# Optimization experiments

Hardware: AMD Instinct MI355X
Metric: run time of the kernel (lower is better)

## Reference

```python
import jax, jax.numpy as jnp
import numpy as np


def conv3x3(x, w):
    # x: [B,C,H,W], w: [O,I,3,3], stride 1, pad 1, no bias
    return jax.lax.conv_general_dilated(
        x, w, window_strides=(1, 1), padding=[(1, 1), (1, 1)],
        dimension_numbers=("NCHW", "OIHW", "NCHW"))


def deform_conv2d(x, offset, w):
    """torchvision-style DeformConv2d: k=3, stride=1, pad=1, dilation=1,
    1 offset group, no bias. x:[B,C,H,W], offset:[B,18,H,W] (dy,dx pairs
    per kernel tap, k = kh*3+kw), w:[O,C,3,3]. Zero padding outside."""
    B, C, H, W = x.shape
    K = 9
    dy = offset[:, 0::2]  # [B,9,H,W]
    dx = offset[:, 1::2]
    kh = (jnp.arange(K) // 3 - 1).astype(x.dtype)[None, :, None, None]
    kw = (jnp.arange(K) % 3 - 1).astype(x.dtype)[None, :, None, None]
    hh = jnp.arange(H, dtype=x.dtype)[None, None, :, None]
    ww = jnp.arange(W, dtype=x.dtype)[None, None, None, :]
    py = hh + kh + dy  # sampling y coord, [B,9,H,W]
    px = ww + kw + dx
    y0 = jnp.floor(py)
    x0 = jnp.floor(px)
    wy = py - y0
    wx = px - x0
    x_hwc = jnp.transpose(x, (0, 2, 3, 1))  # [B,H,W,C]
    b_idx = jnp.arange(B)[:, None, None, None]

    def gather(yi, xi):
        valid = (yi >= 0) & (yi <= H - 1) & (xi >= 0) & (xi <= W - 1)
        yc = jnp.clip(yi, 0, H - 1).astype(jnp.int32)
        xc = jnp.clip(xi, 0, W - 1).astype(jnp.int32)
        v = x_hwc[b_idx, yc, xc]  # [B,9,H,W,C]
        return v * valid[..., None].astype(x.dtype)

    v00 = gather(y0, x0)
    v01 = gather(y0, x0 + 1)
    v10 = gather(y0 + 1, x0)
    v11 = gather(y0 + 1, x0 + 1)
    wy = wy[..., None]
    wx = wx[..., None]
    sampled = (v00 * (1 - wy) * (1 - wx) + v01 * (1 - wy) * wx
               + v10 * wy * (1 - wx) + v11 * wy * wx)  # [B,9,H,W,C]
    wk = w.reshape(w.shape[0], w.shape[1], K)  # [O,C,9]
    return jnp.einsum("bkhwc,ock->bohw", sampled, wk)


def setup_inputs() -> dict:
    key = jax.random.key(0)
    ks = jax.random.split(key, 6)
    B, C, H, W = 2, 128, 128, 128
    s = 0.05  # small init so learned offsets stay in a realistic range
    return {
        "input_features": jax.random.normal(ks[0], (B, C, H, W), jnp.float32),
        "reference_features": jax.random.normal(ks[1], (B, C, H, W), jnp.float32),
        "w_est1": jax.random.normal(ks[2], (C, 2 * C, 3, 3), jnp.float32) * s,
        "w_est2": jax.random.normal(ks[3], (C, C, 3, 3), jnp.float32) * s,
        "w_off": jax.random.normal(ks[4], (18, C, 3, 3), jnp.float32) * s,
        "w_def": jax.random.normal(ks[5], (C, C, 3, 3), jnp.float32) * s,
    }


def reference(input_features, reference_features, w_est1, w_est2, w_off, w_def):
    # concat input+reference features along channel dim
    feat = jnp.concatenate([input_features, reference_features], axis=1)  # [B,2C,H,W]
    # dynamic offset estimator: 2-layer 3x3 conv stack 2C->C->C with ReLU
    est = jax.nn.relu(conv3x3(feat, w_est1))
    est = jax.nn.relu(conv3x3(est, w_est2))
    # offset head: C -> 2*9 offsets per pixel
    offset = conv3x3(est, w_off)  # [B,18,H,W]
    # deformable conv over the reference features
    return deform_conv2d(reference_features, offset, w_def)
```

## Files before the change

kernel.cpp:

```cpp
#include <hip/hip_runtime.h>

typedef _Float16 f16;
typedef __attribute__((ext_vector_type(8))) _Float16 f16x8;
typedef __attribute__((ext_vector_type(4))) float f32x4;

#define H_ 128
#define W_ 128


__device__ __forceinline__ void g2l16(const void* g, void* l) {
  __builtin_amdgcn_global_load_lds((const __attribute__((address_space(1))) void*)g,
                                   (__attribute__((address_space(3))) void*)l, 16, 0, 0);
}

__device__ __forceinline__ void pack_conv(const float* __restrict__ src, f16* __restrict__ dst,
                                          long idx, int C, int NT, int NB, int O) {
  int ci3 = idx & 7;
  int g = (idx >> 3) & 3;
  long t1 = idx >> 5;
  int o = t1 % NT;  long t2 = t1 / NT;
  int kx = t2 % 3;  long t3 = t2 / 3;
  int nb = t3 % NB; long t4 = t3 / NB;
  int nkc = C >> 5;
  int cc = t4 % nkc;
  int ky = t4 / nkc;
  int oo = nb * NT + o;
  int c = (cc << 5) + ((g ^ ((o >> 1) & 3)) << 3) + ci3;
  float v = (oo < O) ? src[(((size_t)oo * C + c) * 3 + ky) * 3 + kx] : 0.f;
  dst[idx] = (f16)v;
}

__device__ __forceinline__ void halo_zero(f16* __restrict__ buf, long e, int C) {
  int c = e & (C - 1);
  long t = e / C;
  int b = (int)(t / 516);
  int p = (int)(t % 516);
  int y, x;
  if (p < 130)      { y = 0;   x = p; }
  else if (p < 260) { y = 129; x = p - 130; }
  else if (p < 388) { x = 0;   y = p - 259; }
  else              { x = 129; y = p - 387; }
  buf[((size_t)(b * 130 + y) * 130 + x) * C + c] = (f16)0.f;
}

__global__ __launch_bounds__(256) void prep_k(const float* __restrict__ w1, const float* __restrict__ w2,
                                              const float* __restrict__ woff, const float* __restrict__ wdef,
                                              f16* __restrict__ W1p, f16* __restrict__ W2p,
                                              f16* __restrict__ Woffp, f16* __restrict__ Wdefp,
                                              f16* __restrict__ featB, f16* __restrict__ est1,
                                              f16* __restrict__ est2) {
  long idx = (long)blockIdx.x * 256 + threadIdx.x;
  if (idx < 294912) { pack_conv(w1, W1p, idx, 256, 64, 2, 128); return; }
  idx -= 294912;
  if (idx < 147456) { pack_conv(w2, W2p, idx, 128, 64, 2, 128); return; }
  idx -= 147456;
  if (idx < 36864) { pack_conv(woff, Woffp, idx, 128, 32, 1, 18); return; }
  idx -= 36864;
  if (idx < 147456) {
    int ci3 = idx & 7;
    int g = (idx >> 3) & 15;
    int o = (idx >> 7) & 127;
    int t = (int)(idx >> 14);
    int c = ((g ^ (o & 7)) << 3) + ci3;
    Wdefp[idx] = (f16)wdef[(((size_t)o * 128 + c) * 3 + t / 3) * 3 + t % 3];
    return;
  }
  idx -= 147456;
  if (idx < 264192) { halo_zero(featB, idx, 256); return; }
  idx -= 264192;
  if (idx < 132096) { halo_zero(est1, idx, 128); return; }
  idx -= 132096;
  if (idx < 132096) halo_zero(est2, idx, 128);
}

__global__ __launch_bounds__(256) void to_nhwc_k(const float* __restrict__ x,
                                                 const float* __restrict__ ref,
                                                 f16* __restrict__ featB) {
  int row = blockIdx.x;
  int b = row >> 7, h = row & 127;
  int w0 = blockIdx.y * 64;
  int chunk = blockIdx.z;
  const float* src = (chunk < 4) ? x : ref;
  int c0 = (chunk & 3) * 32;
  __shared__ __align__(16) f16 T[64][40];
  int tid = threadIdx.x;
#pragma unroll
  for (int i = 0; i < 2; ++i) {
    int idx = tid + i * 256;
    int c = idx >> 4, g = idx & 15;
    const float4 v = *(const float4*)(src + (((size_t)(b * 128 + c0 + c)) * H_ + h) * W_ + w0 + g * 4);
    T[g * 4 + 0][c] = (f16)v.x;
    T[g * 4 + 1][c] = (f16)v.y;
    T[g * 4 + 2][c] = (f16)v.z;
    T[g * 4 + 3][c] = (f16)v.w;
  }
  __syncthreads();
  int w = tid >> 2, g = tid & 3;
  f16x8 o = *(const f16x8*)&T[w][g * 8];
  *(f16x8*)(featB + ((size_t)(b * 130 + h + 1) * 130 + w0 + w + 1) * 256 + chunk * 32 + g * 8) = o;
}

template <int CIN, int NT, bool RELU, bool F16OUT>
__global__ __launch_bounds__(256, 2) void conv_k(const f16* __restrict__ src,
                                                 const f16* __restrict__ Wp,
                                                 f16* __restrict__ dstH,
                                                 float* __restrict__ dstF) {
  const int row = blockIdx.x, nb = blockIdx.y;
  const int b = row >> 7, h = row & 127;
  constexpr int NKC = CIN / 32;
  constexpr int NB = (NT == 64) ? 2 : 1;
  __shared__ __align__(16) f16 As[130][32];
  __shared__ __align__(16) f16 Bs[3][NT][32];
  const int tid = threadIdx.x;
  const int lane = tid & 63, wave = tid >> 6;
  const int l16 = lane & 15, quad = lane >> 4;
  constexpr int MI = (NT == 64) ? 4 : 2;
  const int wmBase = (NT == 64) ? (wave >> 1) * 64 : wave * 32;
  const int wn = (NT == 64) ? (wave & 1) : 0;
  f32x4 acc[MI][2] = {};
  char* AsF = (char*)&As[0][0];
  char* BsF = (char*)&Bs[0][0][0];
  for (int ky = 0; ky < 3; ++ky) {
    const f16* abase0 = src + ((size_t)(b * 130 + h + ky) * 130) * CIN;
    for (int cc = 0; cc < NKC; ++cc) {
      __syncthreads();
      const f16* abase = abase0 + cc * 32;
      {
#pragma unroll
        for (int r = 0; r < 2; ++r) {
          int ch = r * 256 + tid;
          int x = ch >> 2, g = ch & 3;
          g2l16(abase + (size_t)x * CIN + ((g ^ ((x >> 1) & 3)) << 3), AsF + ch * 16);
        }
        if (tid < 8) {
          int ch = 512 + tid;
          int x = ch >> 2, g = ch & 3;
          g2l16(abase + (size_t)x * CIN + ((g ^ ((x >> 1) & 3)) << 3), AsF + ch * 16);
        }
      }
      {
        const f16* bbase = Wp + ((size_t)((ky * NKC + cc) * NB + nb)) * (3 * NT * 32);
        constexpr int BCH = 3 * NT * 32 / 8;
#pragma unroll
        for (int r = 0; r < BCH / 256; ++r) {
          int ch = r * 256 + tid;
          g2l16(bbase + ch * 8, BsF + ch * 16);
        }
        if constexpr (BCH % 256) {
          if (tid < BCH % 256) {
            int ch = (BCH / 256) * 256 + tid;
            g2l16(bbase + ch * 8, BsF + ch * 16);
          }
        }
      }
      __syncthreads();
#pragma unroll
      for (int kx = 0; kx < 3; ++kx) {
        f16x8 bf[2];
#pragma unroll
        for (int j = 0; j < 2; ++j) {
          int o = wn * 32 + j * 16 + l16;
          bf[j] = *(const f16x8*)&Bs[kx][o][(quad ^ ((o >> 1) & 3)) << 3];
        }
#pragma unroll
        for (int i = 0; i < MI; ++i) {
          int x = wmBase + i * 16 + l16 + kx;
          f16x8 a = *(const f16x8*)&As[x][(quad ^ ((x >> 1) & 3)) << 3];
#pragma unroll
          for (int j = 0; j < 2; ++j)
            acc[i][j] = __builtin_amdgcn_mfma_f32_16x16x32_f16(a, bf[j], acc[i][j], 0, 0, 0);
        }
      }
    }
  }
#pragma unroll
  for (int i = 0; i < MI; ++i)
#pragma unroll
    for (int j = 0; j < 2; ++j) {
      int o = nb * NT + wn * 32 + j * 16 + l16;
#pragma unroll
      for (int r = 0; r < 4; ++r) {
        int m = wmBase + i * 16 + quad * 4 + r;
        float v = acc[i][j][r];
        if (RELU) v = fmaxf(v, 0.f);
        if (F16OUT)
          dstH[((size_t)(b * 130 + h + 1) * 130 + m + 1) * 128 + o] = (f16)v;
        else
          dstF[((size_t)row * 128 + m) * 32 + o] = v;
      }
    }
}

__global__ __launch_bounds__(256, 2) void deform_k(const f16* __restrict__ featB,
                                                   const float* __restrict__ offb,
                                                   const f16* __restrict__ Wdefp,
                                                   float* __restrict__ out) {
  const int row = blockIdx.x, tile = blockIdx.y;
  const int b = row >> 7, h = row & 127;
  __shared__ __align__(16) f16 Ws[128][128];
  __shared__ __align__(16) f16 Ss[64][128];
  __shared__ int4 mlds[9][64];
  const int tid = threadIdx.x;
  const int lane = tid & 63, wave = tid >> 6;
  const int l16 = lane & 15, quad = lane >> 4;
  for (int e = tid; e < 576; e += 256) {
    int t = e >> 6, p = e & 63;
    int w = tile * 64 + p;
    const float2 d = *(const float2*)(offb + ((size_t)row * 128 + w) * 32 + 2 * t);
    float py = (float)(h + t / 3 - 1) + d.x;
    float pxf = (float)(w + t % 3 - 1) + d.y;
    float fy = floorf(py), fx = floorf(pxf);
    mlds[t][p] = make_int4((int)fy, (int)fx, __float_as_int(py - fy), __float_as_int(pxf - fx));
  }
  f32x4 acc[2][4] = {};
  const int px = tid >> 2;
  const int cgrp = tid & 3;
  char* WsF = (char*)&Ws[0][0];
  for (int t = 0; t < 9; ++t) {
    __syncthreads();
    const f16* wt = Wdefp + (size_t)t * 16384;
#pragma unroll
    for (int r = 0; r < 8; ++r) {
      int ch = r * 256 + tid;
      g2l16(wt + ch * 8, WsF + ch * 16);
    }
    {
      int4 mt = mlds[t][px];
      int iy = mt.x, ix = mt.y;
      float wy = __int_as_float(mt.z), wx = __int_as_float(mt.w);
      int yp = iy + 1, xp = ix + 1;
      bool y0v = (unsigned)yp < 130u, y1v = (unsigned)(yp + 1) < 130u;
      bool x0v = (unsigned)xp < 130u, x1v = (unsigned)(xp + 1) < 130u;
      int cy0 = y0v ? yp : 0, cy1 = y1v ? yp + 1 : 0;
      int cx0 = x0v ? xp : 0, cx1 = x1v ? xp + 1 : 0;
      float u0 = (1.f - wy) * (y0v ? 1.f : 0.f), u1 = wy * (y1v ? 1.f : 0.f);
      float s0 = (1.f - wx) * (x0v ? 1.f : 0.f), s1 = wx * (x1v ? 1.f : 0.f);
      f16 h00 = (f16)(u0 * s0), h01 = (f16)(u0 * s1);
      f16 h10 = (f16)(u1 * s0), h11 = (f16)(u1 * s1);
      const size_t bb = (size_t)b * 130;
      const f16* p00 = featB + ((bb + cy0) * 130 + cx0) * 256 + 128 + cgrp * 32;
      const f16* p01 = featB + ((bb + cy0) * 130 + cx1) * 256 + 128 + cgrp * 32;
      const f16* p10 = featB + ((bb + cy1) * 130 + cx0) * 256 + 128 + cgrp * 32;
      const f16* p11 = featB + ((bb + cy1) * 130 + cx1) * 256 + 128 + cgrp * 32;
      f16x8 v00[4], v01[4], v10[4], v11[4];
#pragma unroll
      for (int q = 0; q < 4; ++q) {
        v00[q] = *(const f16x8*)(p00 + q * 8);
        v01[q] = *(const f16x8*)(p01 + q * 8);
        v10[q] = *(const f16x8*)(p10 + q * 8);
        v11[q] = *(const f16x8*)(p11 + q * 8);
      }
#pragma unroll
      for (int q = 0; q < 4; ++q) {
        f16x8 rb = v00[q] * h00 + v01[q] * h01 + v10[q] * h10 + v11[q] * h11;
        int c = cgrp * 4 + q;
        *(f16x8*)&Ss[px][(c ^ (px & 7)) << 3] = rb;
      }
    }
    __syncthreads();
#pragma unroll
    for (int cc = 0; cc < 4; ++cc) {
      f16x8 af[2], bf[4];
#pragma unroll
      for (int i = 0; i < 2; ++i) {
        int o = wave * 32 + i * 16 + l16;
        af[i] = *(const f16x8*)&Ws[o][((cc * 4 + quad) ^ (o & 7)) << 3];
      }
#pragma unroll
      for (int j = 0; j < 4; ++j) {
        int p = j * 16 + l16;
        bf[j] = *(const f16x8*)&Ss[p][((cc * 4 + quad) ^ (p & 7)) << 3];
      }
#pragma unroll
      for (int i = 0; i < 2; ++i)
#pragma unroll
        for (int j = 0; j < 4; ++j)
          acc[i][j] = __builtin_amdgcn_mfma_f32_16x16x32_f16(af[i], bf[j], acc[i][j], 0, 0, 0);
    }
  }
#pragma unroll
  for (int i = 0; i < 2; ++i)
#pragma unroll
    for (int r = 0; r < 4; ++r) {
      int o = wave * 32 + i * 16 + quad * 4 + r;
#pragma unroll
      for (int j = 0; j < 4; ++j) {
        int w = tile * 64 + j * 16 + l16;
        out[((size_t)(b * 128 + o) * 128 + h) * 128 + w] = acc[i][j][r];
      }
    }
}

extern "C" void kernel_launch(void* const* d_in, const int* in_sizes, int n_in,
                              void* d_out, int out_size, void* d_ws, size_t ws_size,
                              hipStream_t stream) {
  const float* x = (const float*)d_in[0];
  const float* ref = (const float*)d_in[1];
  const float* w1 = (const float*)d_in[2];
  const float* w2 = (const float*)d_in[3];
  const float* woff = (const float*)d_in[4];
  const float* wdef = (const float*)d_in[5];
  float* out = (float*)d_out;
  char* ws = (char*)d_ws;
  f16* featB = (f16*)(ws + 0);
  f16* est1 = (f16*)(ws + 17305600);
  f16* est2 = (f16*)(ws + 25958400);
  float* offb = (float*)(ws + 34611200);
  f16* W1p = (f16*)(ws + 38805504);
  f16* W2p = (f16*)(ws + 39395328);
  f16* Woffp = (f16*)(ws + 39690240);
  f16* Wdefp = (f16*)(ws + 39763968);

  prep_k<<<dim3(4512), 256, 0, stream>>>(w1, w2, woff, wdef, W1p, W2p, Woffp, Wdefp,
                                         featB, est1, est2);
  to_nhwc_k<<<dim3(256, 2, 8), 256, 0, stream>>>(x, ref, featB);
  conv_k<256, 64, true, true><<<dim3(256, 2), 256, 0, stream>>>(featB, W1p, est1, nullptr);
  conv_k<128, 64, true, true><<<dim3(256, 2), 256, 0, stream>>>(est1, W2p, est2, nullptr);
  conv_k<128, 32, false, false><<<dim3(256, 1), 256, 0, stream>>>(est2, Woffp, nullptr, offb);
  deform_k<<<dim3(256, 2), 256, 0, stream>>>(featB, offb, Wdefp, out);
}
```

Measured before the change: 183.3 us.

## Fuse offset conv into deform kernel, double-buffer convs, merge prep kernels

Merges the NHWC transpose into the weight-prep kernel and removes one launch. The conv kernel is retiled: each block now covers 64 pixels by 128 output channels, with double-buffered LDS staging of activations and weights. The offset-head conv is computed inside the deform kernel with MFMA reading est2 directly, which drops the separate launch and the fp32 offset buffer. The deform kernel splits output channels across a grid z dimension and double-buffers sampling and weight DMA. The trade is that the offset conv is recomputed once per output-channel half, LDS use per block rises, and the offset conv reads its weights straight from global memory.

```diff
diff --git a/kernel.cpp b/kernel.cpp
--- a/kernel.cpp
+++ b/kernel.cpp
@@ -14,20 +14,17 @@
 }
 
 __device__ __forceinline__ void pack_conv(const float* __restrict__ src, f16* __restrict__ dst,
-                                          long idx, int C, int NT, int NB, int O) {
+                                          long idx, int C) {
   int ci3 = idx & 7;
   int g = (idx >> 3) & 3;
   long t1 = idx >> 5;
-  int o = t1 % NT;  long t2 = t1 / NT;
-  int kx = t2 % 3;  long t3 = t2 / 3;
-  int nb = t3 % NB; long t4 = t3 / NB;
+  int o = t1 & 127; t1 >>= 7;
+  int kx = t1 % 3; t1 /= 3;
   int nkc = C >> 5;
-  int cc = t4 % nkc;
-  int ky = t4 / nkc;
-  int oo = nb * NT + o;
+  int cc = t1 % nkc;
+  int ky = (int)(t1 / nkc);
   int c = (cc << 5) + ((g ^ ((o >> 1) & 3)) << 3) + ci3;
-  float v = (oo < O) ? src[(((size_t)oo * C + c) * 3 + ky) * 3 + kx] : 0.f;
-  dst[idx] = (f16)v;
+  dst[idx] = (f16)src[(((size_t)o * C + c) * 3 + ky) * 3 + kx];
 }
 
 __device__ __forceinline__ void halo_zero(f16* __restrict__ buf, long e, int C) {
@@ -43,26 +40,62 @@
   buf[((size_t)(b * 130 + y) * 130 + x) * C + c] = (f16)0.f;
 }
 
-__global__ __launch_bounds__(256) void prep_k(const float* __restrict__ w1, const float* __restrict__ w2,
+__global__ __launch_bounds__(256) void init_k(const float* __restrict__ x, const float* __restrict__ ref,
+                                              const float* __restrict__ w1, const float* __restrict__ w2,
                                               const float* __restrict__ woff, const float* __restrict__ wdef,
                                               f16* __restrict__ W1p, f16* __restrict__ W2p,
                                               f16* __restrict__ Woffp, f16* __restrict__ Wdefp,
                                               f16* __restrict__ featB, f16* __restrict__ est1,
                                               f16* __restrict__ est2) {
-  long idx = (long)blockIdx.x * 256 + threadIdx.x;
-  if (idx < 294912) { pack_conv(w1, W1p, idx, 256, 64, 2, 128); return; }
+  __shared__ __align__(16) f16 T[64][40];
+  int tid = threadIdx.x;
+  if (blockIdx.x < 4096) {
+    int bi = blockIdx.x;
+    int row = bi & 255, wseg = (bi >> 8) & 1, chunk = bi >> 9;
+    int b = row >> 7, h = row & 127;
+    int w0 = wseg * 64;
+    const float* src = (chunk < 4) ? x : ref;
+    int c0 = (chunk & 3) * 32;
+#pragma unroll
+    for (int i = 0; i < 2; ++i) {
+      int idx = tid + i * 256;
+      int c = idx >> 4, g = idx & 15;
+      const float4 v = *(const float4*)(src + (((size_t)(b * 128 + c0 + c)) * H_ + h) * W_ + w0 + g * 4);
+      T[g * 4 + 0][c] = (f16)v.x;
+      T[g * 4 + 1][c] = (f16)v.y;
+      T[g * 4 + 2][c] = (f16)v.z;
+      T[g * 4 + 3][c] = (f16)v.w;
+    }
+    __syncthreads();
+    int w = tid >> 2, g = tid & 3;
+    f16x8 o = *(const f16x8*)&T[w][g * 8];
+    *(f16x8*)(featB + ((size_t)(b * 130 + h + 1) * 130 + w0 + w + 1) * 256 + chunk * 32 + g * 8) = o;
+    return;
+  }
+  long idx = (long)(blockIdx.x - 4096) * 256 + tid;
+  if (idx < 294912) { pack_conv(w1, W1p, idx, 256); return; }
   idx -= 294912;
-  if (idx < 147456) { pack_conv(w2, W2p, idx, 128, 64, 2, 128); return; }
+  if (idx < 147456) { pack_conv(w2, W2p, idx, 128); return; }
   idx -= 147456;
-  if (idx < 36864) { pack_conv(woff, Woffp, idx, 128, 32, 1, 18); return; }
+  if (idx < 36864) {
+    int kk = idx & 31;
+    int o = (int)((idx >> 5) & 31);
+    int rest = (int)(idx >> 10);
+    int cc = rest & 3, kxy = rest >> 2;
+    int ky = kxy / 3, kx = kxy % 3;
+    Woffp[idx] = (o < 18) ? (f16)woff[(((size_t)o * 128 + cc * 32 + kk) * 3 + ky) * 3 + kx] : (f16)0.f;
+    return;
+  }
   idx -= 36864;
   if (idx < 147456) {
     int ci3 = idx & 7;
     int g = (idx >> 3) & 15;
-    int o = (idx >> 7) & 127;
+    int o = (int)((idx >> 7) & 63);
+    int ob = (int)((idx >> 13) & 1);
     int t = (int)(idx >> 14);
     int c = ((g ^ (o & 7)) << 3) + ci3;
-    Wdefp[idx] = (f16)wdef[(((size_t)o * 128 + c) * 3 + t / 3) * 3 + t % 3];
+    int og = ob * 64 + o;
+    Wdefp[idx] = (f16)wdef[(((size_t)og * 128 + c) * 3 + t / 3) * 3 + t % 3];
     return;
   }
   idx -= 147456;
@@ -73,220 +106,208 @@
   if (idx < 132096) halo_zero(est2, idx, 128);
 }
 
-__global__ __launch_bounds__(256) void to_nhwc_k(const float* __restrict__ x,
-                                                 const float* __restrict__ ref,
-                                                 f16* __restrict__ featB) {
-  int row = blockIdx.x;
-  int b = row >> 7, h = row & 127;
-  int w0 = blockIdx.y * 64;
-  int chunk = blockIdx.z;
-  const float* src = (chunk < 4) ? x : ref;
-  int c0 = (chunk & 3) * 32;
-  __shared__ __align__(16) f16 T[64][40];
-  int tid = threadIdx.x;
-#pragma unroll
-  for (int i = 0; i < 2; ++i) {
-    int idx = tid + i * 256;
-    int c = idx >> 4, g = idx & 15;
-    const float4 v = *(const float4*)(src + (((size_t)(b * 128 + c0 + c)) * H_ + h) * W_ + w0 + g * 4);
-    T[g * 4 + 0][c] = (f16)v.x;
-    T[g * 4 + 1][c] = (f16)v.y;
-    T[g * 4 + 2][c] = (f16)v.z;
-    T[g * 4 + 3][c] = (f16)v.w;
-  }
-  __syncthreads();
-  int w = tid >> 2, g = tid & 3;
-  f16x8 o = *(const f16x8*)&T[w][g * 8];
-  *(f16x8*)(featB + ((size_t)(b * 130 + h + 1) * 130 + w0 + w + 1) * 256 + chunk * 32 + g * 8) = o;
-}
-
-template <int CIN, int NT, bool RELU, bool F16OUT>
+template <int CIN>
 __global__ __launch_bounds__(256, 2) void conv_k(const f16* __restrict__ src,
                                                  const f16* __restrict__ Wp,
-                                                 f16* __restrict__ dstH,
-                                                 float* __restrict__ dstF) {
-  const int row = blockIdx.x, nb = blockIdx.y;
-  const int b = row >> 7, h = row & 127;
+                                                 f16* __restrict__ dst) {
   constexpr int NKC = CIN / 32;
-  constexpr int NB = (NT == 64) ? 2 : 1;
-  __shared__ __align__(16) f16 As[130][32];
-  __shared__ __align__(16) f16 Bs[3][NT][32];
+  constexpr int S = 3 * NKC;
+  const int r = blockIdx.x;
+  const int xseg = r & 1, h = (r >> 1) & 127, b = r >> 8;
+  const int x0 = xseg * 64;
+  __shared__ __align__(16) f16 As[2][66][32];
+  __shared__ __align__(16) f16 Bs[2][3][128][32];
   const int tid = threadIdx.x;
   const int lane = tid & 63, wave = tid >> 6;
   const int l16 = lane & 15, quad = lane >> 4;
-  constexpr int MI = (NT == 64) ? 4 : 2;
-  const int wmBase = (NT == 64) ? (wave >> 1) * 64 : wave * 32;
-  const int wn = (NT == 64) ? (wave & 1) : 0;
-  f32x4 acc[MI][2] = {};
-  char* AsF = (char*)&As[0][0];
-  char* BsF = (char*)&Bs[0][0][0];
-  for (int ky = 0; ky < 3; ++ky) {
-    const f16* abase0 = src + ((size_t)(b * 130 + h + ky) * 130) * CIN;
-    for (int cc = 0; cc < NKC; ++cc) {
-      __syncthreads();
-      const f16* abase = abase0 + cc * 32;
-      {
-#pragma unroll
-        for (int r = 0; r < 2; ++r) {
-          int ch = r * 256 + tid;
-          int x = ch >> 2, g = ch & 3;
-          g2l16(abase + (size_t)x * CIN + ((g ^ ((x >> 1) & 3)) << 3), AsF + ch * 16);
-        }
-        if (tid < 8) {
-          int ch = 512 + tid;
-          int x = ch >> 2, g = ch & 3;
-          g2l16(abase + (size_t)x * CIN + ((g ^ ((x >> 1) & 3)) << 3), AsF + ch * 16);
-        }
-      }
-      {
-        const f16* bbase = Wp + ((size_t)((ky * NKC + cc) * NB + nb)) * (3 * NT * 32);
-        constexpr int BCH = 3 * NT * 32 / 8;
-#pragma unroll
-        for (int r = 0; r < BCH / 256; ++r) {
-          int ch = r * 256 + tid;
-          g2l16(bbase + ch * 8, BsF + ch * 16);
-        }
-        if constexpr (BCH % 256) {
-          if (tid < BCH % 256) {
-            int ch = (BCH / 256) * 256 + tid;
-            g2l16(bbase + ch * 8, BsF + ch * 16);
-          }
-        }
-      }
-      __syncthreads();
-#pragma unroll
-      for (int kx = 0; kx < 3; ++kx) {
-        f16x8 bf[2];
-#pragma unroll
-        for (int j = 0; j < 2; ++j) {
-          int o = wn * 32 + j * 16 + l16;
-          bf[j] = *(const f16x8*)&Bs[kx][o][(quad ^ ((o >> 1) & 3)) << 3];
-        }
-#pragma unroll
-        for (int i = 0; i < MI; ++i) {
-          int x = wmBase + i * 16 + l16 + kx;
-          f16x8 a = *(const f16x8*)&As[x][(quad ^ ((x >> 1) & 3)) << 3];
-#pragma unroll
-          for (int j = 0; j < 2; ++j)
-            acc[i][j] = __builtin_amdgcn_mfma_f32_16x16x32_f16(a, bf[j], acc[i][j], 0, 0, 0);
-        }
-      }
-    }
-  }
-#pragma unroll
-  for (int i = 0; i < MI; ++i)
-#pragma unroll
-    for (int j = 0; j < 2; ++j) {
-      int o = nb * NT + wn * 32 + j * 16 + l16;
-#pragma unroll
-      for (int r = 0; r < 4; ++r) {
-        int m = wmBase + i * 16 + quad * 4 + r;
-        float v = acc[i][j][r];
-        if (RELU) v = fmaxf(v, 0.f);
-        if (F16OUT)
-          dstH[((size_t)(b * 130 + h + 1) * 130 + m + 1) * 128 + o] = (f16)v;
-        else
-          dstF[((size_t)row * 128 + m) * 32 + o] = v;
+  const int wmB = (wave & 1) * 32;
+  const int wnB = (wave >> 1) * 64;
+  f32x4 acc[2][4] = {};
+
+  auto stage = [&](int s, int buf) {
+    int ky = s / NKC, cc = s % NKC;
+    const f16* abase = src + ((size_t)(b * 130 + h + ky) * 130 + x0) * CIN + cc * 32;
+    {
+      int xx = tid >> 2, g = tid & 3;
+      g2l16(abase + (size_t)xx * CIN + ((g ^ ((xx >> 1) & 3)) << 3),
+            (char*)&As[buf][0][0] + tid * 16);
+      if (tid < 8) {
+        int ch2 = 256 + tid;
+        int xx2 = ch2 >> 2, g2 = ch2 & 3;
+        g2l16(abase + (size_t)xx2 * CIN + ((g2 ^ ((xx2 >> 1) & 3)) << 3),
+              (char*)&As[buf][0][0] + ch2 * 16);
+      }
+    }
+    const f16* bbase = Wp + (size_t)(ky * NKC + cc) * (3 * 128 * 32);
+#pragma unroll
+    for (int rr = 0; rr < 6; ++rr) {
+      int ch = rr * 256 + tid;
+      g2l16(bbase + (size_t)ch * 8, (char*)&Bs[buf][0][0][0] + ch * 16);
+    }
+  };
+
+  stage(0, 0);
+  __syncthreads();
+  for (int s = 0; s < S; ++s) {
+    if (s + 1 < S) stage(s + 1, (s + 1) & 1);
+    const int buf = s & 1;
+#pragma unroll
+    for (int kx = 0; kx < 3; ++kx) {
+      f16x8 bf[4];
+#pragma unroll
+      for (int j = 0; j < 4; ++j) {
+        int o = wnB + j * 16 + l16;
+        bf[j] = *(const f16x8*)&Bs[buf][kx][o][(quad ^ ((o >> 1) & 3)) << 3];
+      }
+#pragma unroll
+      for (int i = 0; i < 2; ++i) {
+        int xx = wmB + i * 16 + l16 + kx;
+        f16x8 a = *(const f16x8*)&As[buf][xx][(quad ^ ((xx >> 1) & 3)) << 3];
+#pragma unroll
+        for (int j = 0; j < 4; ++j)
+          acc[i][j] = __builtin_amdgcn_mfma_f32_16x16x32_f16(a, bf[j], acc[i][j], 0, 0, 0);
+      }
+    }
+    __syncthreads();
+  }
+#pragma unroll
+  for (int i = 0; i < 2; ++i)
+#pragma unroll
+    for (int j = 0; j < 4; ++j) {
+      int o = wnB + j * 16 + l16;
+#pragma unroll
+      for (int rr = 0; rr < 4; ++rr) {
+        int m = wmB + i * 16 + quad * 4 + rr;
+        float v = fmaxf(acc[i][j][rr], 0.f);
+        dst[((size_t)(b * 130 + h + 1) * 130 + x0 + m + 1) * 128 + o] = (f16)v;
       }
     }
 }
 
 __global__ __launch_bounds__(256, 2) void deform_k(const f16* __restrict__ featB,
-                                                   const float* __restrict__ offb,
+                                                   const f16* __restrict__ est2,
+                                                   const f16* __restrict__ Woffp,
                                                    const f16* __restrict__ Wdefp,
                                                    float* __restrict__ out) {
-  const int row = blockIdx.x, tile = blockIdx.y;
+  const int row = blockIdx.x;
+  const int tile = blockIdx.y;
+  const int ot = blockIdx.z;
   const int b = row >> 7, h = row & 127;
-  __shared__ __align__(16) f16 Ws[128][128];
-  __shared__ __align__(16) f16 Ss[64][128];
-  __shared__ int4 mlds[9][64];
+  __shared__ __align__(16) f16 Wb[2][64][128];
+  __shared__ __align__(16) f16 Ss[2][64][128];
+  __shared__ float offs[64][33];
   const int tid = threadIdx.x;
   const int lane = tid & 63, wave = tid >> 6;
   const int l16 = lane & 15, quad = lane >> 4;
-  for (int e = tid; e < 576; e += 256) {
-    int t = e >> 6, p = e & 63;
-    int w = tile * 64 + p;
-    const float2 d = *(const float2*)(offb + ((size_t)row * 128 + w) * 32 + 2 * t);
-    float py = (float)(h + t / 3 - 1) + d.x;
-    float pxf = (float)(w + t % 3 - 1) + d.y;
+
+  {
+    f32x4 oacc[2] = {};
+    const int pxb = tile * 64 + wave * 16;
+    for (int kxy = 0; kxy < 9; ++kxy) {
+      int ky = kxy / 3, kx = kxy % 3;
+      const f16* arow = est2 + ((size_t)(b * 130 + h + ky) * 130 + pxb + kx) * 128;
+#pragma unroll
+      for (int cc = 0; cc < 4; ++cc) {
+        f16x8 a = *(const f16x8*)(arow + (size_t)l16 * 128 + cc * 32 + quad * 8);
+        const f16* bb = Woffp + ((size_t)(kxy * 4 + cc) * 32 + l16) * 32 + quad * 8;
+        f16x8 b0 = *(const f16x8*)bb;
+        f16x8 b1 = *(const f16x8*)(bb + 16 * 32);
+        oacc[0] = __builtin_amdgcn_mfma_f32_16x16x32_f16(a, b0, oacc[0], 0, 0, 0);
+        oacc[1] = __builtin_amdgcn_mfma_f32_16x16x32_f16(a, b1, oacc[1], 0, 0, 0);
+      }
+    }
+#pragma unroll
+    for (int j = 0; j < 2; ++j)
+#pragma unroll
+      for (int rr = 0; rr < 4; ++rr)
+        offs[wave * 16 + quad * 4 + rr][j * 16 + l16] = oacc[j][rr];
+  }
+  __syncthreads();
+
+  auto wdma = [&](int t, int buf) {
+    const f16* wt = Wdefp + ((size_t)t * 2 + ot) * 8192;
+#pragma unroll
+    for (int rr = 0; rr < 4; ++rr) {
+      int ch = rr * 256 + tid;
+      g2l16(wt + (size_t)ch * 8, (char*)&Wb[buf][0][0] + ch * 16);
+    }
+  };
+  auto sample = [&](int t, int buf) {
+    const int px = tid >> 2, cgrp = tid & 3;
+    float dy = offs[px][2 * t], dx = offs[px][2 * t + 1];
+    int wg = tile * 64 + px;
+    float py = (float)(h + t / 3 - 1) + dy;
+    float pxf = (float)(wg + t % 3 - 1) + dx;
     float fy = floorf(py), fx = floorf(pxf);
-    mlds[t][p] = make_int4((int)fy, (int)fx, __float_as_int(py - fy), __float_as_int(pxf - fx));
-  }
-  f32x4 acc[2][4] = {};
-  const int px = tid >> 2;
-  const int cgrp = tid & 3;
-  char* WsF = (char*)&Ws[0][0];
+    float wy = py - fy, wx = pxf - fx;
+    int yp = (int)fy + 1, xp = (int)fx + 1;
+    bool y0v = (unsigned)yp < 130u, y1v = (unsigned)(yp + 1) < 130u;
+    bool x0v = (unsigned)xp < 130u, x1v = (unsigned)(xp + 1) < 130u;
+    int cy0 = y0v ? yp : 0, cy1 = y1v ? yp + 1 : 0;
+    int cx0 = x0v ? xp : 0, cx1 = x1v ? xp + 1 : 0;
+    float u0 = (1.f - wy) * (y0v ? 1.f : 0.f), u1 = wy * (y1v ? 1.f : 0.f);
+    float s0 = (1.f - wx) * (x0v ? 1.f : 0.f), s1 = wx * (x1v ? 1.f : 0.f);
+    f16 h00 = (f16)(u0 * s0), h01 = (f16)(u0 * s1);
+    f16 h10 = (f16)(u1 * s0), h11 = (f16)(u1 * s1);
+    const size_t bb130 = (size_t)b * 130;
+    const f16* p00 = featB + ((bb130 + cy0) * 130 + cx0) * 256 + 128 + cgrp * 32;
+    const f16* p01 = featB + ((bb130 + cy0) * 130 + cx1) * 256 + 128 + cgrp * 32;
+    const f16* p10 = featB + ((bb130 + cy1) * 130 + cx0) * 256 + 128 + cgrp * 32;
+    const f16* p11 = featB + ((bb130 + cy1) * 130 + cx1) * 256 + 128 + cgrp * 32;
+    f16x8 v00[4], v01[4], v10[4], v11[4];
+#pragma unroll
+    for (int q = 0; q < 4; ++q) {
+      v00[q] = *(const f16x8*)(p00 + q * 8);
+      v01[q] = *(const f16x8*)(p01 + q * 8);
+      v10[q] = *(const f16x8*)(p10 + q * 8);
+      v11[q] = *(const f16x8*)(p11 + q * 8);
+    }
+#pragma unroll
+    for (int q = 0; q < 4; ++q) {
+      f16x8 rb = v00[q] * h00 + v01[q] * h01 + v10[q] * h10 + v11[q] * h11;
+      int c = cgrp * 4 + q;
+      *(f16x8*)&Ss[buf][px][(c ^ (px & 7)) << 3] = rb;
+    }
+  };
+
+  sample(0, 0);
+  wdma(0, 0);
+  __syncthreads();
+  const int wo = wave >> 1, wp = wave & 1;
+  f32x4 acc[2][2] = {};
   for (int t = 0; t < 9; ++t) {
+    if (t < 8) { wdma(t + 1, (t + 1) & 1); sample(t + 1, (t + 1) & 1); }
+    const int buf = t & 1;
+#pragma unroll
+    for (int cc = 0; cc < 4; ++cc) {
+      f16x8 af[2], bf[2];
+#pragma unroll
+      for (int i = 0; i < 2; ++i) {
+        int o = wo * 32 + i * 16 + l16;
+        af[i] = *(const f16x8*)&Wb[buf][o][((cc * 4 + quad) ^ (o & 7)) << 3];
+      }
+#pragma unroll
+      for (int j = 0; j < 2; ++j) {
+        int p = wp * 32 + j * 16 + l16;
+        bf[j] = *(const f16x8*)&Ss[buf][p][((cc * 4 + quad) ^ (p & 7)) << 3];
+      }
+#pragma unroll
+      for (int i = 0; i < 2; ++i)
+#pragma unroll
+        for (int j = 0; j < 2; ++j)
+          acc[i][j] = __builtin_amdgcn_mfma_f32_16x16x32_f16(af[i], bf[j], acc[i][j], 0, 0, 0);
+    }
     __syncthreads();
-    const f16* wt = Wdefp + (size_t)t * 16384;
-#pragma unroll
-    for (int r = 0; r < 8; ++r) {
-      int ch = r * 256 + tid;
-      g2l16(wt + ch * 8, WsF + ch * 16);
-    }
-    {
-      int4 mt = mlds[t][px];
-      int iy = mt.x, ix = mt.y;
-      float wy = __int_as_float(mt.z), wx = __int_as_float(mt.w);
-      int yp = iy + 1, xp = ix + 1;
-      bool y0v = (unsigned)yp < 130u, y1v = (unsigned)(yp + 1) < 130u;
-      bool x0v = (unsigned)xp < 130u, x1v = (unsigned)(xp + 1) < 130u;
-      int cy0 = y0v ? yp : 0, cy1 = y1v ? yp + 1 : 0;
-      int cx0 = x0v ? xp : 0, cx1 = x1v ? xp + 1 : 0;
-      float u0 = (1.f - wy) * (y0v ? 1.f : 0.f), u1 = wy * (y1v ? 1.f : 0.f);
-      float s0 = (1.f - wx) * (x0v ? 1.f : 0.f), s1 = wx * (x1v ? 1.f : 0.f);
-      f16 h00 = (f16)(u0 * s0), h01 = (f16)(u0 * s1);
-      f16 h10 = (f16)(u1 * s0), h11 = (f16)(u1 * s1);
-      const size_t bb = (size_t)b * 130;
-      const f16* p00 = featB + ((bb + cy0) * 130 + cx0) * 256 + 128 + cgrp * 32;
-      const f16* p01 = featB + ((bb + cy0) * 130 + cx1) * 256 + 128 + cgrp * 32;
-      const f16* p10 = featB + ((bb + cy1) * 130 + cx0) * 256 + 128 + cgrp * 32;
-      const f16* p11 = featB + ((bb + cy1) * 130 + cx1) * 256 + 128 + cgrp * 32;
-      f16x8 v00[4], v01[4], v10[4], v11[4];
-#pragma unroll
-      for (int q = 0; q < 4; ++q) {
-        v00[q] = *(const f16x8*)(p00 + q * 8);
-        v01[q] = *(const f16x8*)(p01 + q * 8);
-        v10[q] = *(const f16x8*)(p10 + q * 8);
-        v11[q] = *(const f16x8*)(p11 + q * 8);
-      }
-#pragma unroll
-      for (int q = 0; q < 4; ++q) {
-        f16x8 rb = v00[q] * h00 + v01[q] * h01 + v10[q] * h10 + v11[q] * h11;
-        int c = cgrp * 4 + q;
-        *(f16x8*)&Ss[px][(c ^ (px & 7)) << 3] = rb;
-      }
-    }
-    __syncthreads();
-#pragma unroll
-    for (int cc = 0; cc < 4; ++cc) {
-      f16x8 af[2], bf[4];
-#pragma unroll
-      for (int i = 0; i < 2; ++i) {
-        int o = wave * 32 + i * 16 + l16;
-        af[i] = *(const f16x8*)&Ws[o][((cc * 4 + quad) ^ (o & 7)) << 3];
-      }
-#pragma unroll
-      for (int j = 0; j < 4; ++j) {
-        int p = j * 16 + l16;
-        bf[j] = *(const f16x8*)&Ss[p][((cc * 4 + quad) ^ (p & 7)) << 3];
-      }
-#pragma unroll
-      for (int i = 0; i < 2; ++i)
-#pragma unroll
-        for (int j = 0; j < 4; ++j)
-          acc[i][j] = __builtin_amdgcn_mfma_f32_16x16x32_f16(af[i], bf[j], acc[i][j], 0, 0, 0);
-    }
   }
 #pragma unroll
   for (int i = 0; i < 2; ++i)
 #pragma unroll
-    for (int r = 0; r < 4; ++r) {
-      int o = wave * 32 + i * 16 + quad * 4 + r;
-#pragma unroll
-      for (int j = 0; j < 4; ++j) {
-        int w = tile * 64 + j * 16 + l16;
-        out[((size_t)(b * 128 + o) * 128 + h) * 128 + w] = acc[i][j][r];
+    for (int rr = 0; rr < 4; ++rr) {
+      int og = ot * 64 + wo * 32 + i * 16 + quad * 4 + rr;
+#pragma unroll
+      for (int j = 0; j < 2; ++j) {
+        int wg = tile * 64 + wp * 32 + j * 16 + l16;
+        out[((size_t)(b * 128 + og) * 128 + h) * 128 + wg] = acc[i][j][rr];
       }
     }
 }
@@ -305,17 +326,14 @@
   f16* featB = (f16*)(ws + 0);
   f16* est1 = (f16*)(ws + 17305600);
   f16* est2 = (f16*)(ws + 25958400);
-  float* offb = (float*)(ws + 34611200);
-  f16* W1p = (f16*)(ws + 38805504);
-  f16* W2p = (f16*)(ws + 39395328);
-  f16* Woffp = (f16*)(ws + 39690240);
-  f16* Wdefp = (f16*)(ws + 39763968);
-
-  prep_k<<<dim3(4512), 256, 0, stream>>>(w1, w2, woff, wdef, W1p, W2p, Woffp, Wdefp,
-                                         featB, est1, est2);
-  to_nhwc_k<<<dim3(256, 2, 8), 256, 0, stream>>>(x, ref, featB);
-  conv_k<256, 64, true, true><<<dim3(256, 2), 256, 0, stream>>>(featB, W1p, est1, nullptr);
-  conv_k<128, 64, true, true><<<dim3(256, 2), 256, 0, stream>>>(est1, W2p, est2, nullptr);
-  conv_k<128, 32, false, false><<<dim3(256, 1), 256, 0, stream>>>(est2, Woffp, nullptr, offb);
-  deform_k<<<dim3(256, 2), 256, 0, stream>>>(featB, offb, Wdefp, out);
-}
+  f16* W1p = (f16*)(ws + 34611200);
+  f16* W2p = (f16*)(ws + 35201024);
+  f16* Woffp = (f16*)(ws + 35495936);
+  f16* Wdefp = (f16*)(ws + 35569664);
+
+  init_k<<<dim3(8608), 256, 0, stream>>>(x, ref, w1, w2, woff, wdef,
+                                         W1p, W2p, Woffp, Wdefp, featB, est1, est2);
+  conv_k<256><<<dim3(512), 256, 0, stream>>>(featB, W1p, est1);
+  conv_k<128><<<dim3(512), 256, 0, stream>>>(est1, W2p, est2);
+  deform_k<<<dim3(256, 2, 2), 256, 0, stream>>>(featB, est2, Woffp, Wdefp, out);
+}
```

New measurement: 218.2 us. 19.0% more time.
